# Kernel tuning notes

Hardware: AMD Instinct MI355X
Metric: run time of the kernel (lower is better)

## Reference

```python
import jax, jax.numpy as jnp
import numpy as np

N_QUBITS = 8


def _zsign(n):
    # sign of PauliZ eigenvalue for each basis state on each wire; wire 0 is MSB
    idx = np.arange(2 ** n)
    bits = (idx[:, None] >> (n - 1 - np.arange(n))) & 1
    return jnp.asarray(1.0 - 2.0 * bits, dtype=jnp.float32)  # (2^n, n)


ZSIGN = _zsign(N_QUBITS)


def qgate(angles):
    """Simulate: RX(angle_w) per wire (encoder RX + trainable RX already summed,
    since RX(a)RX(b)=RX(a+b)), CNOT chain, then <Z_w> per wire.
    angles: (B, n) real -> (B, n) expectation values in [-1, 1]."""
    B, n = angles.shape
    c = jnp.cos(angles / 2).astype(jnp.complex64)
    s = (-1j * jnp.sin(angles / 2)).astype(jnp.complex64)
    # product state |psi> = kron_w [cos(a/2), -i sin(a/2)], wire 0 = MSB
    state = jnp.ones((B, 1), jnp.complex64)
    for w in range(n):
        qs = jnp.stack([c[:, w], s[:, w]], axis=-1)  # (B, 2)
        state = (state[:, :, None] * qs[:, None, :]).reshape(B, -1)
    # CNOT chain on wires (i, i+1)
    for i in range(n - 1):
        d0, d1 = 2 ** i, 2 ** (n - i - 2)
        st = state.reshape(B, d0, 2, 2, d1)
        st = jnp.stack([st[:, :, 0], st[:, :, 1, ::-1]], axis=2)
        state = st.reshape(B, -1)
    probs = state.real ** 2 + state.imag ** 2  # (B, 2^n)
    return probs @ ZSIGN  # (B, n)


def setup_inputs() -> dict:
    key = jax.random.key(0)
    S, B, D, H = 256, 256, 256, N_QUBITS
    fan = D + H
    ks = jax.random.split(key, 13)
    inputs = jax.random.normal(ks[0], (S, B, D), dtype=jnp.float32)
    hx = jnp.zeros((B, H), jnp.float32)
    cx = jnp.zeros((B, H), jnp.float32)
    bound = 1.0 / np.sqrt(fan)

    def lin(kw, kb):
        W = jax.random.uniform(kw, (H, fan), minval=-bound, maxval=bound, dtype=jnp.float32)
        b = jax.random.uniform(kb, (H,), minval=-bound, maxval=bound, dtype=jnp.float32)
        return W, b

    Wf, bf = lin(ks[1], ks[2])
    Wi, bi = lin(ks[3], ks[4])
    Wu, bu = lin(ks[5], ks[6])
    Wo, bo = lin(ks[7], ks[8])
    theta_f = jax.random.normal(ks[9], (H,), dtype=jnp.float32) * 0.1
    theta_i = jax.random.normal(ks[10], (H,), dtype=jnp.float32) * 0.1
    theta_u = jax.random.normal(ks[11], (H,), dtype=jnp.float32) * 0.1
    theta_o = jax.random.normal(ks[12], (H,), dtype=jnp.float32) * 0.1
    return {"inputs": inputs, "hx": hx, "cx": cx,
            "Wf": Wf, "bf": bf, "Wi": Wi, "bi": bi,
            "Wu": Wu, "bu": bu, "Wo": Wo, "bo": bo,
            "theta_f": theta_f, "theta_i": theta_i,
            "theta_u": theta_u, "theta_o": theta_o}


def reference(inputs, hx, cx, Wf, bf, Wi, bi, Wu, bu, Wo, bo,
              theta_f, theta_i, theta_u, theta_o):
    def step(carry, x):
        h, c = carry
        z = jnp.concatenate([x, h], axis=1)  # (B, D+H)
        f = jax.nn.sigmoid(qgate(z @ Wf.T + bf + theta_f))
        i = jax.nn.sigmoid(qgate(z @ Wi.T + bi + theta_i))
        g = jnp.tanh(qgate(z @ Wu.T + bu + theta_u))
        o = jax.nn.sigmoid(qgate(z @ Wo.T + bo + theta_o))
        c = f * c + i * g
        h = o * jnp.tanh(c)
        return (h, c), h

    (hT, cT), outs = jax.lax.scan(step, (hx, cx), inputs)
    return outs, hT, cT
```

## Files before the change

### kernel.cpp

```cpp
#include <hip/hip_runtime.h>


#define S_LEN 256
#define BATCH 256
#define DIMK  256
#define FAN   264
#define CHUNK 32
#define NCH   8
#define NKV   4
#define TPB   320

__device__ __forceinline__ float lo16f(unsigned u) {
    union { unsigned u; float f; } v; v.u = u << 16; return v.f;
}
__device__ __forceinline__ float hi16f(unsigned u) {
    union { unsigned u; float f; } v; v.u = u & 0xffff0000u; return v.f;
}
__device__ __forceinline__ float b2f(unsigned short u) {
    union { unsigned u; float f; } v; v.u = ((unsigned)u) << 16; return v.f;
}
__device__ __forceinline__ unsigned short f2b(float f) {
    union { float f; unsigned u; } v; v.f = f;
    unsigned r = v.u + 0x7fffu + ((v.u >> 16) & 1u);
    return (unsigned short)(r >> 16);
}
__device__ __forceinline__ float sane(float x) {
    return (__builtin_fabsf(x) < 1e30f) ? x : 0.f;
}
__device__ __forceinline__ float ldE(const void* p, int idx, bool f32) {
    return f32 ? ((const float*)p)[idx] : b2f(((const unsigned short*)p)[idx]);
}
__device__ __forceinline__ void stE(void* p, long idx, float v, bool f32) {
    if (f32) ((float*)p)[idx] = v;
    else     ((unsigned short*)p)[idx] = f2b(v);
}

template<int CTRL>
__device__ __forceinline__ float dpp_f(float x) {
    int xi = __builtin_bit_cast(int, x);
    int r = __builtin_amdgcn_update_dpp(xi, xi, CTRL, 0xF, 0xF, false);
    return __builtin_bit_cast(float, r);
}
template<int IMM>
__device__ __forceinline__ float swz_f(float x) {
    return __builtin_bit_cast(float,
        __builtin_amdgcn_ds_swizzle(__builtin_bit_cast(int, x), IMM));
}
__device__ __forceinline__ float rdlane_f(float x, int l) {
    return __builtin_bit_cast(float,
        __builtin_amdgcn_readlane(__builtin_bit_cast(int, x), l));
}

__global__ __launch_bounds__(TPB, 1) void qlstm_fused(
    const void* __restrict__ X,  const void* __restrict__ hx, const void* __restrict__ cx,
    const void* __restrict__ Wf, const void* __restrict__ bf_,
    const void* __restrict__ Wi, const void* __restrict__ bi_,
    const void* __restrict__ Wu, const void* __restrict__ bu_,
    const void* __restrict__ Wo, const void* __restrict__ bo_,
    const void* __restrict__ tf, const void* __restrict__ ti,
    const void* __restrict__ tu, const void* __restrict__ to_,
    void* __restrict__ out)
{
    __shared__ float As4[2][NKV][CHUNK][32];
    __shared__ int s_isf32;

    const int tid = threadIdx.x;
    const int b   = blockIdx.x;

    if (tid == 0) {
        const unsigned short* u = (const unsigned short*)X;
        int hits = 0;
        for (int i = 0; i < 64; ++i) {
            int e = (u[2 * i] >> 7) & 0xFF;
            if (e >= 110 && e <= 135) ++hits;
        }
        s_isf32 = (hits < 32) ? 1 : 0;
    }
    __syncthreads();
    const bool f32 = (s_isf32 != 0);

    const int wv   = tid >> 6;
    const int lane = tid & 63;
    const int kv   = wv - 1;
    const int o    = lane & 31;
    const int th   = lane >> 5;
    const int g    = o >> 3, w = o & 7;
    const void* Wg = (g == 0) ? Wf : (g == 1) ? Wi : (g == 2) ? Wu : Wo;

    float4 wreg[16];
    if (wv >= 1) {
        if (f32) {
            const float4* wr =
                (const float4*)((const float*)Wg + w * FAN + kv * 64);
#pragma unroll
            for (int i = 0; i < 16; ++i) wreg[i] = wr[i];
        } else {
            const uint4* wr =
                (const uint4*)((const unsigned short*)Wg + w * FAN + kv * 64);
#pragma unroll
            for (int i = 0; i < 8; ++i) {
                uint4 wu = wr[i];
                wreg[2 * i + 0] = make_float4(lo16f(wu.x), hi16f(wu.x),
                                              lo16f(wu.y), hi16f(wu.y));
                wreg[2 * i + 1] = make_float4(lo16f(wu.z), hi16f(wu.z),
                                              lo16f(wu.w), hi16f(wu.w));
            }
        }
    }

    auto fill = [&](int ch) {
        float (*dst)[32] = As4[ch & 1][kv];
        const int tb = ch * CHUNK + th * 16;
        if (f32) {
            for (int j = 0; j < 16; ++j) {
                const float4* xr = (const float4*)((const float*)X
                        + ((long)(tb + j) * BATCH + b) * DIMK + kv * 64);
                float a0 = 0.f, a1 = 0.f, a2 = 0.f, a3 = 0.f;
#pragma unroll
                for (int i = 0; i < 16; ++i) {
                    float4 xu = xr[i];
                    a0 = fmaf(xu.x, wreg[i].x, a0);
                    a1 = fmaf(xu.y, wreg[i].y, a1);
                    a2 = fmaf(xu.z, wreg[i].z, a2);
                    a3 = fmaf(xu.w, wreg[i].w, a3);
                }
                dst[th * 16 + j][o] = sane((a0 + a1) + (a2 + a3));
            }
        } else {
            for (int j = 0; j < 16; ++j) {
                const uint4* xr = (const uint4*)((const unsigned short*)X
                        + ((long)(tb + j) * BATCH + b) * DIMK + kv * 64);
                float a0 = 0.f, a1 = 0.f, a2 = 0.f, a3 = 0.f;
#pragma unroll
                for (int i = 0; i < 8; ++i) {
                    uint4 xu = xr[i];
                    a0 = fmaf(lo16f(xu.x), wreg[2 * i].x, a0);
                    a1 = fmaf(hi16f(xu.x), wreg[2 * i].y, a1);
                    a2 = fmaf(lo16f(xu.y), wreg[2 * i].z, a2);
                    a3 = fmaf(hi16f(xu.y), wreg[2 * i].w, a3);
                    a0 = fmaf(lo16f(xu.z), wreg[2 * i + 1].x, a0);
                    a1 = fmaf(hi16f(xu.z), wreg[2 * i + 1].y, a1);
                    a2 = fmaf(lo16f(xu.w), wreg[2 * i + 1].z, a2);
                    a3 = fmaf(hi16f(xu.w), wreg[2 * i + 1].w, a3);
                }
                dst[th * 16 + j][o] = sane((a0 + a1) + (a2 + a3));
            }
        }
    };

    float Wh[8];
    float bt = 0.f, h = 0.f, c = 0.f, qv = 1.f;
    int rw = 0, rg = 0;
    if (tid < 32) {
        rw = tid & 7; rg = tid >> 3;
        const void* bg = (rg == 0) ? bf_ : (rg == 1) ? bi_ : (rg == 2) ? bu_ : bo_;
        const void* tg = (rg == 0) ? tf  : (rg == 1) ? ti  : (rg == 2) ? tu  : to_;
        const int wr = rw * FAN;
#pragma unroll
        for (int j = 0; j < 8; ++j)
            Wh[j] = sane(ldE(Wg, wr + DIMK + j, f32));
        bt = sane(ldE(bg, rw, f32)) + sane(ldE(tg, rw, f32));
        h  = sane(ldE(hx, b * 8 + rw, f32));
        c  = sane(ldE(cx, b * 8 + rw, f32));
        qv = (rg == 2) ? 2.f : 1.f;
    }
    if (wv == 0) __builtin_amdgcn_s_setprio(1);

    if (wv >= 1) fill(0);
    __syncthreads();

    for (int ch = 0; ch < NCH; ++ch) {
        if (wv >= 1 && ch + 1 < NCH) fill(ch + 1);
        if (tid < 32) {
            const int buf = ch & 1;
            float n0 = As4[buf][0][0][tid], n1 = As4[buf][1][0][tid];
            float n2 = As4[buf][2][0][tid], n3 = As4[buf][3][0][tid];
            float a_cur = (n0 + n1) + (n2 + n3);
            for (int s = 0; s < CHUNK; ++s) {
                const int sn = (s < CHUNK - 1) ? s + 1 : s;
                float m0 = As4[buf][0][sn][tid], m1 = As4[buf][1][sn][tid];
                float m2 = As4[buf][2][sn][tid], m3 = As4[buf][3][sn][tid];

                float d0 = 0.f, d1 = 0.f;
#pragma unroll
                for (int j = 0; j < 8; j += 2) {
                    d0 = fmaf(rdlane_f(h, j),     Wh[j],     d0);
                    d1 = fmaf(rdlane_f(h, j + 1), Wh[j + 1], d1);
                }
                float ang = a_cur + bt + (d0 + d1);
                float e = __cosf(ang);

                { float v = dpp_f<0x111>(e); e = (rw >= 1) ? e * v : e; }
                { float v = dpp_f<0x112>(e); e = (rw >= 2) ? e * v : e; }
                { float v = dpp_f<0x114>(e); e = (rw >= 4) ? e * v : e; }

                float ez  = __expf(qv * e);
                float val = 1.f - __fdividef(qv, ez + 1.f);

                float fg = swz_f<0x007>(val);
                float ig = swz_f<0x107>(val);
                float ug = swz_f<0x207>(val);
                float og = swz_f<0x307>(val);

                c = fmaf(fg, c, ig * ug);
                float e2 = __expf(2.f * c);
                float th2 = 1.f - __fdividef(2.f, e2 + 1.f);
                h = og * th2;

                if (rg == 0)
                    stE(out, (long)(ch * CHUNK + s) * 2048 + b * 8 + rw, h, f32);
                a_cur = (m0 + m1) + (m2 + m3);
            }
        }
        __syncthreads();
    }

    if (tid < 32 && rg == 0) {
        stE(out, 524288L + b * 8 + rw, h, f32);
        stE(out, 526336L + b * 8 + rw, c, f32);
    }
}

extern "C" void kernel_launch(void* const* d_in, const int* in_sizes, int n_in,
                              void* d_out, int out_size, void* d_ws, size_t ws_size,
                              hipStream_t stream) {
    qlstm_fused<<<dim3(BATCH), dim3(TPB), 0, stream>>>(
        d_in[0], d_in[1], d_in[2],
        d_in[3], d_in[4], d_in[5], d_in[6],
        d_in[7], d_in[8], d_in[9], d_in[10],
        d_in[11], d_in[12], d_in[13], d_in[14],
        d_out);
}
```

Baseline: 213.9 us.

## Split into parallel input-projection GEMM and lightweight batched recurrence kernel

```diff
diff --git a/kernel.cpp b/kernel.cpp
--- a/kernel.cpp
+++ b/kernel.cpp
@@ -5,10 +5,8 @@
 #define BATCH 256
 #define DIMK  256
 #define FAN   264
-#define CHUNK 32
-#define NCH   8
-#define NKV   4
-#define TPB   320
+#define NROWS (S_LEN * BATCH)
+#define WS_NEED ((size_t)NROWS * 32 * 4)
 
 __device__ __forceinline__ float lo16f(unsigned u) {
     union { unsigned u; float f; } v; v.u = u << 16; return v.f;
@@ -33,6 +31,12 @@
 __device__ __forceinline__ void stE(void* p, long idx, float v, bool f32) {
     if (f32) ((float*)p)[idx] = v;
     else     ((unsigned short*)p)[idx] = f2b(v);
+}
+__device__ __forceinline__ float sigm(float x) {
+    return 1.f - __fdividef(1.f, __expf(x) + 1.f);
+}
+__device__ __forceinline__ float tanh_f(float x) {
+    return 1.f - __fdividef(2.f, __expf(2.f * x) + 1.f);
 }
 
 template<int CTRL>
@@ -51,7 +55,187 @@
         __builtin_amdgcn_readlane(__builtin_bit_cast(int, x), l));
 }
 
-__global__ __launch_bounds__(TPB, 1) void qlstm_fused(
+__device__ __forceinline__ int sniff_f32(const void* X) {
+    const unsigned short* u = (const unsigned short*)X;
+    int hits = 0;
+    for (int i = 0; i < 64; ++i) {
+        int e = (u[2 * i] >> 7) & 0xFF;
+        if (e >= 110 && e <= 135) ++hits;
+    }
+    return (hits < 32) ? 1 : 0;
+}
+
+__global__ __launch_bounds__(256, 4) void qlstm_gemm(
+    const void* __restrict__ X,
+    const void* __restrict__ Wf, const void* __restrict__ Wi,
+    const void* __restrict__ Wu, const void* __restrict__ Wo,
+    float* __restrict__ A)
+{
+    __shared__ float red[4][64][32];
+    __shared__ int s_isf32;
+
+    const int tid = threadIdx.x;
+    if (tid == 0) s_isf32 = sniff_f32(X);
+    __syncthreads();
+    const bool f32 = (s_isf32 != 0);
+
+    const int kv = tid >> 6;
+    const int l  = tid & 63;
+    const int o  = l & 31;
+    const int th = l >> 5;
+    const int g  = o >> 3, w = o & 7;
+    const void* Wg = (g == 0) ? Wf : (g == 1) ? Wi : (g == 2) ? Wu : Wo;
+
+    float4 wreg[16];
+    if (f32) {
+        const float4* wr = (const float4*)((const float*)Wg + w * FAN + kv * 64);
+#pragma unroll
+        for (int i = 0; i < 16; ++i) wreg[i] = wr[i];
+    } else {
+        const uint4* wr = (const uint4*)((const unsigned short*)Wg + w * FAN + kv * 64);
+#pragma unroll
+        for (int i = 0; i < 8; ++i) {
+            uint4 wu = wr[i];
+            wreg[2 * i + 0] = make_float4(lo16f(wu.x), hi16f(wu.x),
+                                          lo16f(wu.y), hi16f(wu.y));
+            wreg[2 * i + 1] = make_float4(lo16f(wu.z), hi16f(wu.z),
+                                          lo16f(wu.w), hi16f(wu.w));
+        }
+    }
+
+    const long rowbase = (long)blockIdx.x * 64;
+    for (int j = 0; j < 32; ++j) {
+        const int rl = th * 32 + j;
+        const long row = rowbase + rl;
+        const int t = (int)(row & 255), bb = (int)(row >> 8);
+        float a0 = 0.f, a1 = 0.f, a2 = 0.f, a3 = 0.f;
+        if (f32) {
+            const float4* xr = (const float4*)((const float*)X
+                    + ((long)t * BATCH + bb) * DIMK + kv * 64);
+#pragma unroll
+            for (int i = 0; i < 16; ++i) {
+                float4 xu = xr[i];
+                a0 = fmaf(xu.x, wreg[i].x, a0);
+                a1 = fmaf(xu.y, wreg[i].y, a1);
+                a2 = fmaf(xu.z, wreg[i].z, a2);
+                a3 = fmaf(xu.w, wreg[i].w, a3);
+            }
+        } else {
+            const uint4* xr = (const uint4*)((const unsigned short*)X
+                    + ((long)t * BATCH + bb) * DIMK + kv * 64);
+#pragma unroll
+            for (int i = 0; i < 8; ++i) {
+                uint4 xu = xr[i];
+                a0 = fmaf(lo16f(xu.x), wreg[2 * i].x, a0);
+                a1 = fmaf(hi16f(xu.x), wreg[2 * i].y, a1);
+                a2 = fmaf(lo16f(xu.y), wreg[2 * i].z, a2);
+                a3 = fmaf(hi16f(xu.y), wreg[2 * i].w, a3);
+                a0 = fmaf(lo16f(xu.z), wreg[2 * i + 1].x, a0);
+                a1 = fmaf(hi16f(xu.z), wreg[2 * i + 1].y, a1);
+                a2 = fmaf(lo16f(xu.w), wreg[2 * i + 1].z, a2);
+                a3 = fmaf(hi16f(xu.w), wreg[2 * i + 1].w, a3);
+            }
+        }
+        red[kv][rl][o] = (a0 + a1) + (a2 + a3);
+    }
+    __syncthreads();
+    for (int idx = tid; idx < 64 * 32; idx += 256) {
+        const int rl = idx >> 5, oo = idx & 31;
+        float s = red[0][rl][oo] + red[1][rl][oo]
+                + red[2][rl][oo] + red[3][rl][oo];
+        A[(rowbase + rl) * 32 + oo] = sane(s);
+    }
+}
+
+__global__ __launch_bounds__(64) void qlstm_rec(
+    const void* __restrict__ X,  const void* __restrict__ hx, const void* __restrict__ cx,
+    const void* __restrict__ Wf, const void* __restrict__ bf_,
+    const void* __restrict__ Wi, const void* __restrict__ bi_,
+    const void* __restrict__ Wu, const void* __restrict__ bu_,
+    const void* __restrict__ Wo, const void* __restrict__ bo_,
+    const void* __restrict__ tf, const void* __restrict__ ti,
+    const void* __restrict__ tu, const void* __restrict__ to_,
+    void* __restrict__ out, const float* __restrict__ A)
+{
+    __shared__ int s_isf32;
+    const int tid = threadIdx.x;
+    if (tid == 0) s_isf32 = sniff_f32(X);
+    __syncthreads();
+    const bool f32 = (s_isf32 != 0);
+
+    const int w     = tid & 7;
+    const int bglob = blockIdx.x * 8 + (tid >> 3);
+
+    const void* Wg_[4] = { Wf, Wi, Wu, Wo };
+    const void* bg_[4] = { bf_, bi_, bu_, bo_ };
+    const void* tg_[4] = { tf, ti, tu, to_ };
+
+    float Wh[4][8], bt[4];
+#pragma unroll
+    for (int g = 0; g < 4; ++g) {
+#pragma unroll
+        for (int j = 0; j < 8; ++j)
+            Wh[g][j] = sane(ldE(Wg_[g], w * FAN + DIMK + j, f32));
+        bt[g] = sane(ldE(bg_[g], w, f32)) + sane(ldE(tg_[g], w, f32));
+    }
+    float h = sane(ldE(hx, bglob * 8 + w, f32));
+    float c = sane(ldE(cx, bglob * 8 + w, f32));
+
+    auto cumprod8 = [&](float e) {
+        { float v = dpp_f<0x111>(e); e = (w >= 1) ? e * v : e; }
+        { float v = dpp_f<0x112>(e); e = (w >= 2) ? e * v : e; }
+        { float v = dpp_f<0x114>(e); e = (w >= 4) ? e * v : e; }
+        return e;
+    };
+
+    auto ldA = [&](int t, int g) {
+        return A[(((long)bglob << 8) | t) * 32 + g * 8 + w];
+    };
+
+    auto STEP = [&](int t, float aF, float aI, float aU, float aO) {
+        float hj[8];
+        hj[0] = swz_f<0x038>(h); hj[1] = swz_f<0x058>(h);
+        hj[2] = swz_f<0x078>(h); hj[3] = swz_f<0x098>(h);
+        hj[4] = swz_f<0x0B8>(h); hj[5] = swz_f<0x0D8>(h);
+        hj[6] = swz_f<0x0F8>(h); hj[7] = swz_f<0x118>(h);
+        float angF = aF + bt[0], angI = aI + bt[1];
+        float angU = aU + bt[2], angO = aO + bt[3];
+#pragma unroll
+        for (int j = 0; j < 8; ++j) {
+            angF = fmaf(hj[j], Wh[0][j], angF);
+            angI = fmaf(hj[j], Wh[1][j], angI);
+            angU = fmaf(hj[j], Wh[2][j], angU);
+            angO = fmaf(hj[j], Wh[3][j], angO);
+        }
+        float Ef = cumprod8(__cosf(angF));
+        float Ei = cumprod8(__cosf(angI));
+        float Eu = cumprod8(__cosf(angU));
+        float Eo = cumprod8(__cosf(angO));
+        float vf = sigm(Ef), vi = sigm(Ei), vu = tanh_f(Eu), vo = sigm(Eo);
+        c = fmaf(vf, c, vi * vu);
+        h = vo * tanh_f(c);
+        stE(out, (long)t * 2048 + bglob * 8 + w, h, f32);
+    };
+
+    float aF0 = ldA(0, 0), aI0 = ldA(0, 1), aU0 = ldA(0, 2), aO0 = ldA(0, 3);
+    float aF1 = ldA(1, 0), aI1 = ldA(1, 1), aU1 = ldA(1, 2), aO1 = ldA(1, 3);
+    for (int t = 0; t < S_LEN; t += 2) {
+        const int tp2 = (t + 2 < S_LEN) ? t + 2 : S_LEN - 1;
+        const int tp3 = (t + 3 < S_LEN) ? t + 3 : S_LEN - 1;
+        float nF0 = ldA(tp2, 0), nI0 = ldA(tp2, 1);
+        float nU0 = ldA(tp2, 2), nO0 = ldA(tp2, 3);
+        STEP(t, aF0, aI0, aU0, aO0);
+        float nF1 = ldA(tp3, 0), nI1 = ldA(tp3, 1);
+        float nU1 = ldA(tp3, 2), nO1 = ldA(tp3, 3);
+        STEP(t + 1, aF1, aI1, aU1, aO1);
+        aF0 = nF0; aI0 = nI0; aU0 = nU0; aO0 = nO0;
+        aF1 = nF1; aI1 = nI1; aU1 = nU1; aO1 = nO1;
+    }
+    stE(out, 524288L + bglob * 8 + w, h, f32);
+    stE(out, 526336L + bglob * 8 + w, c, f32);
+}
+
+__global__ __launch_bounds__(320, 1) void qlstm_fused_v6(
     const void* __restrict__ X,  const void* __restrict__ hx, const void* __restrict__ cx,
     const void* __restrict__ Wf, const void* __restrict__ bf_,
     const void* __restrict__ Wi, const void* __restrict__ bi_,
@@ -61,21 +245,13 @@
     const void* __restrict__ tu, const void* __restrict__ to_,
     void* __restrict__ out)
 {
-    __shared__ float As4[2][NKV][CHUNK][32];
+    __shared__ float As4[2][4][32][32];
     __shared__ int s_isf32;
 
     const int tid = threadIdx.x;
     const int b   = blockIdx.x;
 
-    if (tid == 0) {
-        const unsigned short* u = (const unsigned short*)X;
-        int hits = 0;
-        for (int i = 0; i < 64; ++i) {
-            int e = (u[2 * i] >> 7) & 0xFF;
-            if (e >= 110 && e <= 135) ++hits;
-        }
-        s_isf32 = (hits < 32) ? 1 : 0;
-    }
+    if (tid == 0) s_isf32 = sniff_f32(X);
     __syncthreads();
     const bool f32 = (s_isf32 != 0);
 
@@ -90,13 +266,11 @@
     float4 wreg[16];
     if (wv >= 1) {
         if (f32) {
-            const float4* wr =
-                (const float4*)((const float*)Wg + w * FAN + kv * 64);
+            const float4* wr = (const float4*)((const float*)Wg + w * FAN + kv * 64);
 #pragma unroll
             for (int i = 0; i < 16; ++i) wreg[i] = wr[i];
         } else {
-            const uint4* wr =
-                (const uint4*)((const unsigned short*)Wg + w * FAN + kv * 64);
+            const uint4* wr = (const uint4*)((const unsigned short*)Wg + w * FAN + kv * 64);
 #pragma unroll
             for (int i = 0; i < 8; ++i) {
                 uint4 wu = wr[i];
@@ -110,7 +284,7 @@
 
     auto fill = [&](int ch) {
         float (*dst)[32] = As4[ch & 1][kv];
-        const int tb = ch * CHUNK + th * 16;
+        const int tb = ch * 32 + th * 16;
         if (f32) {
             for (int j = 0; j < 16; ++j) {
                 const float4* xr = (const float4*)((const float*)X
@@ -169,18 +343,17 @@
     if (wv >= 1) fill(0);
     __syncthreads();
 
-    for (int ch = 0; ch < NCH; ++ch) {
-        if (wv >= 1 && ch + 1 < NCH) fill(ch + 1);
+    for (int ch = 0; ch < 8; ++ch) {
+        if (wv >= 1 && ch + 1 < 8) fill(ch + 1);
         if (tid < 32) {
             const int buf = ch & 1;
             float n0 = As4[buf][0][0][tid], n1 = As4[buf][1][0][tid];
             float n2 = As4[buf][2][0][tid], n3 = As4[buf][3][0][tid];
             float a_cur = (n0 + n1) + (n2 + n3);
-            for (int s = 0; s < CHUNK; ++s) {
-                const int sn = (s < CHUNK - 1) ? s + 1 : s;
+            for (int s = 0; s < 32; ++s) {
+                const int sn = (s < 31) ? s + 1 : s;
                 float m0 = As4[buf][0][sn][tid], m1 = As4[buf][1][sn][tid];
                 float m2 = As4[buf][2][sn][tid], m3 = As4[buf][3][sn][tid];
-
                 float d0 = 0.f, d1 = 0.f;
 #pragma unroll
                 for (int j = 0; j < 8; j += 2) {
@@ -189,26 +362,21 @@
                 }
                 float ang = a_cur + bt + (d0 + d1);
                 float e = __cosf(ang);
-
                 { float v = dpp_f<0x111>(e); e = (rw >= 1) ? e * v : e; }
                 { float v = dpp_f<0x112>(e); e = (rw >= 2) ? e * v : e; }
                 { float v = dpp_f<0x114>(e); e = (rw >= 4) ? e * v : e; }
-
                 float ez  = __expf(qv * e);
                 float val = 1.f - __fdividef(qv, ez + 1.f);
-
                 float fg = swz_f<0x007>(val);
                 float ig = swz_f<0x107>(val);
                 float ug = swz_f<0x207>(val);
                 float og = swz_f<0x307>(val);
-
                 c = fmaf(fg, c, ig * ug);
                 float e2 = __expf(2.f * c);
                 float th2 = 1.f - __fdividef(2.f, e2 + 1.f);
                 h = og * th2;
-
                 if (rg == 0)
-                    stE(out, (long)(ch * CHUNK + s) * 2048 + b * 8 + rw, h, f32);
+                    stE(out, (long)(ch * 32 + s) * 2048 + b * 8 + rw, h, f32);
                 a_cur = (m0 + m1) + (m2 + m3);
             }
         }
@@ -224,10 +392,21 @@
 extern "C" void kernel_launch(void* const* d_in, const int* in_sizes, int n_in,
                               void* d_out, int out_size, void* d_ws, size_t ws_size,
                               hipStream_t stream) {
-    qlstm_fused<<<dim3(BATCH), dim3(TPB), 0, stream>>>(
-        d_in[0], d_in[1], d_in[2],
-        d_in[3], d_in[4], d_in[5], d_in[6],
-        d_in[7], d_in[8], d_in[9], d_in[10],
-        d_in[11], d_in[12], d_in[13], d_in[14],
-        d_out);
-}
+    if (d_ws != nullptr && ws_size >= WS_NEED) {
+        qlstm_gemm<<<dim3(NROWS / 64), dim3(256), 0, stream>>>(
+            d_in[0], d_in[3], d_in[5], d_in[7], d_in[9], (float*)d_ws);
+        qlstm_rec<<<dim3(BATCH / 8), dim3(64), 0, stream>>>(
+            d_in[0], d_in[1], d_in[2],
+            d_in[3], d_in[4], d_in[5], d_in[6],
+            d_in[7], d_in[8], d_in[9], d_in[10],
+            d_in[11], d_in[12], d_in[13], d_in[14],
+            d_out, (const float*)d_ws);
+    } else {
+        qlstm_fused_v6<<<dim3(BATCH), dim3(320), 0, stream>>>(
+            d_in[0], d_in[1], d_in[2],
+            d_in[3], d_in[4], d_in[5], d_in[6],
+            d_in[7], d_in[8], d_in[9], d_in[10],
+            d_in[11], d_in[12], d_in[13], d_in[14],
+            d_out);
+    }
+}
```

Result: slower. 308.5 us (+44.2%).
